# Performance work log

Measured on AMD Instinct MI355X. Metric: run time of the kernel, lower is better.

## Reference

```python
import jax, jax.numpy as jnp
import numpy as np

N = 50000          # nodes
DEG = 8            # per-node in/out degree
E = N * DEG        # fwd edges (rev = reversed fwd)
H = 128            # hidden_dim
T = 4              # towers
F = H // T         # per-tower F_in (divide_input=True)
FO = H // T        # per-tower F_out
L = 2              # num_layers
IN_DIM = 128
OUT_DIM = 32
AVG_LOG = float(np.log(DEG + 1.0))  # avg of log(deg+1) from deg histogram (all deg==8)
BN_EPS = 1e-5
STD_EPS = 1e-5


def setup_inputs() -> dict:
    key = jax.random.key(0)
    ks = jax.random.split(key, 10)
    x = jax.random.normal(ks[0], (N, IN_DIM), jnp.float32)
    # every node appears exactly DEG times as dst and as src -> deg histogram delta at 8
    dst = jnp.repeat(jnp.arange(N, dtype=jnp.int32), DEG)
    src = jax.random.permutation(ks[1], dst)
    edge_fwd = jnp.stack([src, dst])  # [2, E]

    def rn(k, shape):
        return jax.random.normal(k, shape, jnp.float32) * 0.05

    return dict(
        x=x,
        W_in=rn(ks[2], (IN_DIM, H)), b_in=jnp.zeros((H,), jnp.float32),
        # [layer, relation(fwd/rev), tower, ...]
        pre_W=rn(ks[3], (L, 2, T, 2 * F, F)), pre_b=jnp.zeros((L, 2, T, F), jnp.float32),
        post_W=rn(ks[4], (L, 2, T, 13 * F, FO)), post_b=jnp.zeros((L, 2, T, FO), jnp.float32),
        lin_W=rn(ks[5], (L, 2, H, H)), lin_b=jnp.zeros((L, 2, H), jnp.float32),
        bn_gamma=jnp.ones((L, H), jnp.float32), bn_beta=jnp.zeros((L, H), jnp.float32),
        mlp_W1=rn(ks[6], (H, H)), mlp_b1=jnp.zeros((H,), jnp.float32),
        mlp_W2=rn(ks[7], (H, OUT_DIM)), mlp_b2=jnp.zeros((OUT_DIM,), jnp.float32),
        edge_fwd=edge_fwd,
    )


def _pna(x, src, dst, pre_W, pre_b, post_W, post_b, lin_W, lin_b):
    """One PNAConv (divide_input=True, pre/post_layers=1, no edge attr)."""
    xt = x.reshape(N, T, F)                                   # [N,T,F]
    # message: cat([x_i (dst), x_j (src)]) -> per-tower pre-MLP
    h = jnp.concatenate([xt[dst], xt[src]], axis=-1)          # [E,T,2F]
    m = jnp.einsum('etf,tfg->etg', h, pre_W) + pre_b          # [E,T,F]
    # multi-aggregator scatter reduce over destination nodes
    deg = jax.ops.segment_sum(jnp.ones((m.shape[0],), x.dtype), dst, N)
    degc = jnp.maximum(deg, 1.0)
    inv = (1.0 / degc)[:, None, None]
    mean = jax.ops.segment_sum(m, dst, N) * inv
    mean2 = jax.ops.segment_sum(m * m, dst, N) * inv
    std = jnp.sqrt(jax.nn.relu(mean2 - mean * mean) + STD_EPS)
    mn = jax.ops.segment_min(m, dst, N)
    mx = jax.ops.segment_max(m, dst, N)
    agg = jnp.concatenate([mean, mn, mx, std], axis=-1)       # [N,T,4F]
    # degree scalers: amplification, attenuation, identity
    ld = jnp.log(degc + 1.0)[:, None, None]
    agg = jnp.concatenate([agg * (ld / AVG_LOG), agg * (AVG_LOG / ld), agg], axis=-1)  # [N,T,12F]
    out = jnp.concatenate([xt, agg], axis=-1)                 # [N,T,13F]
    out = jnp.einsum('ntf,tfg->ntg', out, post_W) + post_b    # [N,T,FO]
    out = out.reshape(N, T * FO)
    return out @ lin_W + lin_b                                # [N,H]


def _bn(x, g, b):
    mu = x.mean(0)
    var = x.var(0)  # biased, as torch BatchNorm normalization
    return g * (x - mu) * jax.lax.rsqrt(var + BN_EPS) + b


def reference(x, W_in, b_in, pre_W, pre_b, post_W, post_b, lin_W, lin_b,
              bn_gamma, bn_beta, mlp_W1, mlp_b1, mlp_W2, mlp_b2, edge_fwd):
    src, dst = edge_fwd[0], edge_fwd[1]
    h = jax.nn.relu(x @ W_in + b_in)
    for l in range(L):
        # HeteroConv sum of fwd relation and rev relation (reversed edges)
        y = (_pna(h, src, dst, pre_W[l, 0], pre_b[l, 0], post_W[l, 0], post_b[l, 0], lin_W[l, 0], lin_b[l, 0])
             + _pna(h, dst, src, pre_W[l, 1], pre_b[l, 1], post_W[l, 1], post_b[l, 1], lin_W[l, 1], lin_b[l, 1]))
        h = jax.nn.relu(_bn(y, bn_gamma[l], bn_beta[l]))
        # dropout omitted (deterministic reference / eval mode)
    return jax.nn.relu(h @ mlp_W1 + mlp_b1) @ mlp_W2 + mlp_b2
```

## Files before the change

kernel.cpp:

```cpp
#include <hip/hip_runtime.h>
#include <hip/hip_fp16.h>
#include <cstddef>
#include <cstdint>

#define NN 50000
#define DEG 8
#define EE (NN*DEG)
#define RT_CNT 3125
#define KSTEPS 36
#define W8L 18432
#define MPAD 132

typedef __attribute__((ext_vector_type(8))) short short8;
typedef __attribute__((ext_vector_type(4))) float f32x4;

union Pack8 { __half h[8]; __half2 h2[4]; uint4 u; short8 s8; };

__global__ void k_build_nbr(const int* __restrict__ ef, int* __restrict__ cnt,
                            int* __restrict__ fwd_nbr, int* __restrict__ rev_nbr) {
    int e = blockIdx.x * blockDim.x + threadIdx.x;
    if (e >= EE) return;
    int s = ef[e], d = ef[EE + e];
    int p = atomicAdd(&cnt[d], 1);
    fwd_nbr[d * DEG + p] = s;
    int q = atomicAdd(&cnt[NN + s], 1);
    rev_nbr[s * DEG + q] = d;
}

__global__ __launch_bounds__(256) void k_wprep(
    const float* __restrict__ post_W, const float* __restrict__ pre_W,
    const float* __restrict__ pre_b, const float* __restrict__ post_b,
    const float* __restrict__ lin_W, const float* __restrict__ lin_b,
    __half* __restrict__ Wcp, float* __restrict__ Qw, float* __restrict__ bc) {
    __shared__ float Pf[160 * 33];
    __shared__ float Wl[32 * 128];
    __shared__ float Wt[32 * 32];
    __shared__ float Ps[32 * 32];
    __shared__ float Q[32 * 32];
    __shared__ float T3s[32];
    int tid = threadIdx.x;
    int m4 = blockIdx.x;
    int l = m4 >> 3, r = (m4 >> 2) & 1, tw = m4 & 3;
    const float* PW = post_W + (size_t)m4 * 416 * 32;
    for (int i = tid; i < 160 * 32; i += 256) {
        int row = i >> 5, g = i & 31;
        float v;
        if (row < 32) v = PW[row * 32 + g];
        else {
            int rr = row - 32;
            v = PW[(32 + rr) * 32 + g] + PW[(160 + rr) * 32 + g] + PW[(288 + rr) * 32 + g];
        }
        Pf[row * 33 + g] = v;
    }
    for (int i = tid; i < 1024; i += 256) Wt[i] = pre_W[(size_t)m4 * 2048 + i];
    for (int i = tid; i < 4096; i += 256)
        Wl[i] = lin_W[(size_t)(l * 2 + r) * 16384 + tw * 32 * 128 + i];
    __syncthreads();
    for (int i = tid; i < 1024; i += 256) {
        int g = i >> 5, j = i & 31;
        Ps[i] = Pf[(32 + g) * 33 + j] + Pf[(64 + g) * 33 + j] + Pf[(96 + g) * 33 + j];
    }
    __syncthreads();
    for (int i = tid; i < 1024; i += 256) {
        int f = i >> 5, j = i & 31;
        float acc = Pf[f * 33 + j];
#pragma unroll
        for (int g = 0; g < 32; g++) acc += Wt[f * 32 + g] * Ps[g * 32 + j];
        Q[i] = acc;
    }
    if (tid < 32) {
        int j = tid;
        float v = post_b[m4 * 32 + j];
#pragma unroll
        for (int g = 0; g < 32; g++) v += pre_b[m4 * 32 + g] * Ps[g * 32 + j];
        T3s[j] = v;
    }
    __syncthreads();
    for (int u = tid; u < 2048; u += 256) {
        int lane = u & 63, t = (u >> 6) & 7, s = u >> 9;
        int quad = lane >> 4, nl = lane & 15;
        int n = t * 16 + nl;
        Pack8 pk;
#pragma unroll
        for (int e = 0; e < 8; e++) {
            int f = quad * 8 + e;
            const float* Pr = &Pf[((s + 1) * 32 + f) * 33];
            float acc = 0.f;
#pragma unroll
            for (int j = 0; j < 32; j++) acc += Pr[j] * Wl[j * 128 + n];
            pk.h[e] = __float2half(acc);
        }
        int ks = 4 + r * 16 + tw * 4 + s;
        *(uint4*)&Wcp[((size_t)l * W8L + (t * KSTEPS + ks) * 64 + lane) * 8] = pk.u;
    }
    for (int i = tid; i < 4096; i += 256) {
        int f = i >> 7, n = i & 127;
        float acc = 0.f;
#pragma unroll
        for (int j = 0; j < 32; j++) acc += Q[f * 32 + j] * Wl[j * 128 + n];
        atomicAdd(&Qw[(size_t)l * 16384 + (tw * 32 + f) * 128 + n], acc);
    }
    if (tid < 128) {
        float v = 0.f;
#pragma unroll
        for (int j = 0; j < 32; j++) v += T3s[j] * Wl[j * 128 + tid];
        atomicAdd(&bc[l * 128 + tid], v);
        if ((m4 & 7) == 0)
            atomicAdd(&bc[l * 128 + tid],
                      lin_b[(2 * l) * 128 + tid] + lin_b[(2 * l + 1) * 128 + tid]);
    }
}

__global__ void k_pack_xt(const float* __restrict__ Qw, __half* __restrict__ Wcp) {
    int gid = blockIdx.x * blockDim.x + threadIdx.x;
    if (gid >= 2 * 4 * 8 * 64) return;
    int lane = gid & 63, t = (gid >> 6) & 7, ks = (gid >> 9) & 3, l = gid >> 11;
    int quad = lane >> 4;
    int n = t * 16 + (lane & 15);
    Pack8 pk;
#pragma unroll
    for (int e = 0; e < 8; e++)
        pk.h[e] = __float2half(Qw[(size_t)l * 16384 + (ks * 32 + quad * 8 + e) * 128 + n]);
    *(uint4*)&Wcp[((size_t)l * W8L + (t * KSTEPS + ks) * 64 + lane) * 8] = pk.u;
}

__global__ void k_pack_b(const float* __restrict__ W, int K, int N,
                         __half* __restrict__ dst) {
    int gid = blockIdx.x * blockDim.x + threadIdx.x;
    int total = (K >> 5) * (N >> 4) * 64;
    if (gid >= total) return;
    int lane = gid & 63;
    int ks = (gid >> 6) % (K >> 5);
    int t = (gid >> 6) / (K >> 5);
    int quad = lane >> 4, nl = lane & 15;
    int n = t * 16 + nl;
    Pack8 pk;
#pragma unroll
    for (int e = 0; e < 8; e++)
        pk.h[e] = __float2half(W[(size_t)(ks * 32 + quad * 8 + e) * N + n]);
    *(uint4*)&dst[(size_t)gid * 8] = pk.u;
}

__global__ void k_pack_wbd(const float* __restrict__ pre_W, __half* __restrict__ dst) {
    int gid = blockIdx.x * blockDim.x + threadIdx.x;
    if (gid >= 2 * 2 * 8 * 4 * 64) return;
    int lane = gid & 63, ks = (gid >> 6) & 3, t8 = (gid >> 8) & 7;
    int rel = (gid >> 11) & 1, l = gid >> 12;
    int quad = lane >> 4, nl = lane & 15;
    int n = t8 * 16 + nl;
    int tn = n >> 5;
    Pack8 pk;
#pragma unroll
    for (int e = 0; e < 8; e++) {
        int k = ks * 32 + quad * 8 + e;
        float v = 0.f;
        if ((k >> 5) == tn)
            v = pre_W[(size_t)((((l * 2 + rel) * 4 + tn) * 64) + 32 + (k & 31)) * 32 + (n & 31)];
        pk.h[e] = __float2half(v);
    }
    *(uint4*)&dst[((size_t)(l * 2 + rel) * 2048 + (t8 * 4 + ks) * 64 + lane) * 8] = pk.u;
}

__global__ __launch_bounds__(256) void k_in_fused(
    const float* __restrict__ X, const __half* __restrict__ Wp,
    const float* __restrict__ b, const __half* __restrict__ WbBDp,
    __half* __restrict__ H, __half* __restrict__ Bplanes) {
    __shared__ __half Sh[4][16 * MPAD];
    int tid = threadIdx.x, wv = tid >> 6, lane = tid & 63;
    int rt = blockIdx.x * 4 + wv;
    if (rt >= RT_CNT) rt = RT_CNT - 1;
    int mm = lane & 15, quad = lane >> 4;
    short8 a[4];
#pragma unroll
    for (int ks = 0; ks < 4; ks++) {
        const float4* p = (const float4*)&X[(size_t)(rt * 16 + mm) * 128 + ks * 32 + quad * 8];
        float4 v0 = p[0], v1 = p[1];
        Pack8 pk;
        pk.h[0] = __float2half(v0.x); pk.h[1] = __float2half(v0.y);
        pk.h[2] = __float2half(v0.z); pk.h[3] = __float2half(v0.w);
        pk.h[4] = __float2half(v1.x); pk.h[5] = __float2half(v1.y);
        pk.h[6] = __float2half(v1.z); pk.h[7] = __float2half(v1.w);
        a[ks] = pk.s8;
    }
    const short8* Bb = (const short8*)Wp + lane;
    f32x4 acc[8];
#pragma unroll
    for (int t = 0; t < 8; t++) acc[t] = (f32x4){0.f, 0.f, 0.f, 0.f};
#pragma unroll
    for (int ks = 0; ks < 4; ks++)
#pragma unroll
        for (int t = 0; t < 8; t++)
            acc[t] = __builtin_amdgcn_mfma_f32_16x16x32_f16(
                a[ks], Bb[(t * 4 + ks) * 64], acc[t], 0, 0, 0);
    __half* T = Sh[wv];
#pragma unroll
    for (int t = 0; t < 8; t++) {
        int n = t * 16 + mm;
        float bias = b[n];
#pragma unroll
        for (int r = 0; r < 4; r++)
            T[(quad * 4 + r) * MPAD + n] = __float2half(fmaxf(acc[t][r] + bias, 0.f));
    }
#pragma unroll
    for (int it = 0; it < 4; it++) {
        int idx = it * 64 + lane;
        int row = idx >> 4, col = (idx & 15) * 8;
        *(uint4*)&H[(size_t)(rt * 16 + row) * 128 + col] = *(uint4*)&T[row * MPAD + col];
    }
    short8 a2[4];
#pragma unroll
    for (int ks = 0; ks < 4; ks++)
        a2[ks] = *(const short8*)&T[mm * MPAD + ks * 32 + quad * 8];
#pragma unroll
    for (int rel = 0; rel < 2; rel++) {
        const short8* Bd = (const short8*)WbBDp + (size_t)rel * 2048 + lane;
        f32x4 ac[8];
#pragma unroll
        for (int t = 0; t < 8; t++) ac[t] = (f32x4){0.f, 0.f, 0.f, 0.f};
#pragma unroll
        for (int ks = 0; ks < 4; ks++)
#pragma unroll
            for (int t = 0; t < 8; t++)
                ac[t] = __builtin_amdgcn_mfma_f32_16x16x32_f16(
                    a2[ks], Bd[(t * 4 + ks) * 64], ac[t], 0, 0, 0);
#pragma unroll
        for (int t = 0; t < 8; t++) {
            int n = t * 16 + mm;
#pragma unroll
            for (int r = 0; r < 4; r++)
                T[(quad * 4 + r) * MPAD + n] = __float2half(ac[t][r]);
        }
        __half* Bp = Bplanes + (size_t)rel * NN * 128;
#pragma unroll
        for (int it = 0; it < 4; it++) {
            int idx = it * 64 + lane;
            int row = idx >> 4, col = (idx & 15) * 8;
            *(uint4*)&Bp[(size_t)(rt * 16 + row) * 128 + col] = *(uint4*)&T[row * MPAD + col];
        }
    }
}

template<int V>
__global__ __launch_bounds__(256) void k_preB_mfma(
    const __half* __restrict__ Hin, const float* __restrict__ Yf,
    const float* __restrict__ bns, const float* __restrict__ bns2,
    const float* __restrict__ gamma, const float* __restrict__ beta,
    __half* __restrict__ Hout, const __half* __restrict__ WbBDp,
    __half* __restrict__ Bplanes) {
    __shared__ __half Sh[4][16 * MPAD];
    __shared__ float sc[128], sh[128];
    int tid = threadIdx.x, wv = tid >> 6, lane = tid & 63;
    int rt = blockIdx.x * 4 + wv;
    if (rt >= RT_CNT) rt = RT_CNT - 1;
    if (V == 2) {
        if (tid < 128) {
            float mu = bns[tid] * (1.f / NN);
            float var = bns2[tid] * (1.f / NN) - mu * mu;
            float s = gamma[tid] * rsqrtf(var + 1e-5f);
            sc[tid] = s;
            sh[tid] = beta[tid] - mu * s;
        }
        __syncthreads();
    }
    int mm = lane & 15, quad = lane >> 4;
    short8 a[4];
#pragma unroll
    for (int ks = 0; ks < 4; ks++) {
        int c0 = ks * 32 + quad * 8;
        size_t base = (size_t)(rt * 16 + mm) * 128 + c0;
        if (V == 1) {
            Pack8 pk; pk.u = *(const uint4*)&Hin[base];
            a[ks] = pk.s8;
        } else {
            const float4* p = (const float4*)&Yf[base];
            float4 v0 = p[0], v1 = p[1];
            float4 s0 = *(const float4*)&sc[c0], s1 = *(const float4*)&sc[c0 + 4];
            float4 f0 = *(const float4*)&sh[c0], f1 = *(const float4*)&sh[c0 + 4];
            Pack8 pk;
            pk.h[0] = __float2half(fmaxf(s0.x * v0.x + f0.x, 0.f));
            pk.h[1] = __float2half(fmaxf(s0.y * v0.y + f0.y, 0.f));
            pk.h[2] = __float2half(fmaxf(s0.z * v0.z + f0.z, 0.f));
            pk.h[3] = __float2half(fmaxf(s0.w * v0.w + f0.w, 0.f));
            pk.h[4] = __float2half(fmaxf(s1.x * v1.x + f1.x, 0.f));
            pk.h[5] = __float2half(fmaxf(s1.y * v1.y + f1.y, 0.f));
            pk.h[6] = __float2half(fmaxf(s1.z * v1.z + f1.z, 0.f));
            pk.h[7] = __float2half(fmaxf(s1.w * v1.w + f1.w, 0.f));
            *(uint4*)&Hout[base] = pk.u;
            a[ks] = pk.s8;
        }
    }
    __half* T = Sh[wv];
#pragma unroll
    for (int rel = 0; rel < 2; rel++) {
        const short8* Bb = (const short8*)WbBDp + (size_t)rel * 2048 + lane;
        f32x4 acc[8];
#pragma unroll
        for (int t = 0; t < 8; t++) acc[t] = (f32x4){0.f, 0.f, 0.f, 0.f};
#pragma unroll
        for (int ks = 0; ks < 4; ks++)
#pragma unroll
            for (int t = 0; t < 8; t++)
                acc[t] = __builtin_amdgcn_mfma_f32_16x16x32_f16(
                    a[ks], Bb[(t * 4 + ks) * 64], acc[t], 0, 0, 0);
#pragma unroll
        for (int t = 0; t < 8; t++) {
            int n = t * 16 + mm;
#pragma unroll
            for (int r = 0; r < 4; r++)
                T[(quad * 4 + r) * MPAD + n] = __float2half(acc[t][r]);
        }
        __half* Bp = Bplanes + (size_t)rel * NN * 128;
#pragma unroll
        for (int it = 0; it < 4; it++) {
            int idx = it * 64 + lane;
            int row = idx >> 4, col = (idx & 15) * 8;
            *(uint4*)&Bp[(size_t)(rt * 16 + row) * 128 + col] = *(uint4*)&T[row * MPAD + col];
        }
    }
}

__global__ __launch_bounds__(256, 5) void k_agg_gemm(
    const __half* __restrict__ hbuf, const __half* __restrict__ Bplanes,
    const int* __restrict__ fwd_nbr, const int* __restrict__ rev_nbr,
    const __half* __restrict__ Wcp, const float* __restrict__ bc,
    float* __restrict__ Y, float* __restrict__ bnsum, float* __restrict__ bnsum2) {
    __shared__ __half Spack[32 * 64 * 8];
    int tid = threadIdx.x;
    int blk = blockIdx.x;
    int lane = tid & 63, wv = tid >> 6;
    int s = lane >> 4, f16 = lane & 15;
    int tw = f16 >> 2, quad = f16 & 3;
    int m = wv * 4 + s;
    int d = blk * 16 + m;
    int mB = lane & 15, qB = lane >> 4;
    Pack8 axt[4];
#pragma unroll
    for (int ks = 0; ks < 4; ks++)
        axt[ks].u = *(const uint4*)&hbuf[(size_t)(blk * 16 + mB) * 128 + ks * 32 + qB * 8];
    {
        const int4* nf = (const int4*)&fwd_nbr[d * 8];
        const int4* nr = (const int4*)&rev_nbr[d * 8];
        int4 a0 = nf[0], a1 = nf[1], b0v = nr[0], b1v = nr[1];
        int idx0[8] = {a0.x, a0.y, a0.z, a0.w, a1.x, a1.y, a1.z, a1.w};
        int idx1[8] = {b0v.x, b0v.y, b0v.z, b0v.w, b1v.x, b1v.y, b1v.z, b1v.w};
        int fo = f16 * 8;
        Pack8 r0[8], r1[8];
        const __half* Bp1 = Bplanes + (size_t)NN * 128;
#pragma unroll
        for (int k = 0; k < 8; k++)
            r0[k].u = *(const uint4*)&Bplanes[(size_t)idx0[k] * 128 + fo];
#pragma unroll
        for (int k = 0; k < 8; k++)
            r1[k].u = *(const uint4*)&Bp1[(size_t)idx1[k] * 128 + fo];
        int pos = 16 * quad + (m ^ quad ^ ((tw & 1) << 2));
#pragma unroll
        for (int rel = 0; rel < 2; rel++) {
            Pack8* rr = rel ? r1 : r0;
            float sS[8], qS[8], mnS[8], mxS[8];
#pragma unroll
            for (int j = 0; j < 8; j++) {
                sS[j] = 0.f; qS[j] = 0.f; mnS[j] = 1e30f; mxS[j] = -1e30f;
            }
#pragma unroll
            for (int k = 0; k < 8; k++) {
#pragma unroll
                for (int j2 = 0; j2 < 4; j2++) {
                    __half2 h = rr[k].h2[j2];
                    float a = __half2float(__low2half(h));
                    float b = __half2float(__high2half(h));
                    int j0 = 2 * j2, j1 = j0 + 1;
                    sS[j0] += a; qS[j0] += a * a;
                    mnS[j0] = fminf(mnS[j0], a); mxS[j0] = fmaxf(mxS[j0], a);
                    sS[j1] += b; qS[j1] += b * b;
                    mnS[j1] = fminf(mnS[j1], b); mxS[j1] = fmaxf(mxS[j1], b);
                }
            }
            Pack8 mean, stdv, mnp, mxp;
#pragma unroll
            for (int j = 0; j < 8; j++) {
                float Bm = sS[j] * 0.125f;
                mean.h[j] = __float2half(Bm);
                stdv.h[j] = __float2half(
                    sqrtf(fmaxf(qS[j] * 0.125f - Bm * Bm, 0.f) + 1e-5f));
                mnp.h[j] = __float2half(mnS[j]);
                mxp.h[j] = __float2half(mxS[j]);
            }
            int ksb = rel * 16 + tw * 4;
            *(uint4*)&Spack[((size_t)(ksb + 0) * 64 + pos) * 8] = mean.u;
            *(uint4*)&Spack[((size_t)(ksb + 1) * 64 + pos) * 8] = mnp.u;
            *(uint4*)&Spack[((size_t)(ksb + 2) * 64 + pos) * 8] = mxp.u;
            *(uint4*)&Spack[((size_t)(ksb + 3) * 64 + pos) * 8] = stdv.u;
        }
    }
    __syncthreads();
    int t0 = wv * 2;
    const short8* Bb = (const short8*)Wcp + lane;
    f32x4 acc0 = (f32x4){0.f, 0.f, 0.f, 0.f};
    f32x4 acc1 = (f32x4){0.f, 0.f, 0.f, 0.f};
    short8 p0[6], p1[6];
#pragma unroll
    for (int dd = 0; dd < 6; dd++) {
        p0[dd] = Bb[((size_t)t0 * KSTEPS + dd) * 64];
        p1[dd] = Bb[((size_t)(t0 + 1) * KSTEPS + dd) * 64];
    }
    __builtin_amdgcn_s_setprio(1);
#pragma unroll
    for (int ks = 0; ks < KSTEPS; ks++) {
        short8 a;
        if (ks < 4) {
            a = axt[ks].s8;
        } else {
            int ss = ks - 4;
            int twk = (ss >> 2) & 3;
            int posr = 16 * qB + (mB ^ qB ^ ((twk & 1) << 2));
            a = *(const short8*)&Spack[((size_t)ss * 64 + posr) * 8];
        }
        acc0 = __builtin_amdgcn_mfma_f32_16x16x32_f16(a, p0[ks % 6], acc0, 0, 0, 0);
        acc1 = __builtin_amdgcn_mfma_f32_16x16x32_f16(a, p1[ks % 6], acc1, 0, 0, 0);
        if (ks + 6 < KSTEPS) {
            p0[ks % 6] = Bb[((size_t)t0 * KSTEPS + ks + 6) * 64];
            p1[ks % 6] = Bb[((size_t)(t0 + 1) * KSTEPS + ks + 6) * 64];
        }
    }
    __builtin_amdgcn_s_setprio(0);
#pragma unroll
    for (int tt = 0; tt < 2; tt++) {
        f32x4 acc = tt ? acc1 : acc0;
        int n = (t0 + tt) * 16 + mB;
        float bias = bc[n];
        float ls = 0.f, ls2 = 0.f;
#pragma unroll
        for (int r = 0; r < 4; r++) {
            float v = acc[r] + bias;
            int node = blk * 16 + qB * 4 + r;
            Y[(size_t)node * 128 + n] = v;
            ls += v; ls2 += v * v;
        }
        ls += __shfl_xor(ls, 16); ls += __shfl_xor(ls, 32);
        ls2 += __shfl_xor(ls2, 16); ls2 += __shfl_xor(ls2, 32);
        if (qB == 0) {
            atomicAdd(&bnsum[n], ls);
            atomicAdd(&bnsum2[n], ls2);
        }
    }
}

__global__ __launch_bounds__(256) void k_mlp_mfma(
    const float* __restrict__ Yb, const float* __restrict__ bns,
    const float* __restrict__ bns2, const float* __restrict__ gamma,
    const float* __restrict__ beta, const __half* __restrict__ W1p,
    const float* __restrict__ b1, const __half* __restrict__ W2p,
    const float* __restrict__ b2, float* __restrict__ out) {
    __shared__ __half Sh[4][16 * MPAD];
    __shared__ float sc[128], sh[128];
    int tid = threadIdx.x, wv = tid >> 6, lane = tid & 63;
    int rt = blockIdx.x * 4 + wv;
    if (rt >= RT_CNT) rt = RT_CNT - 1;
    if (tid < 128) {
        float mu = bns[tid] * (1.f / NN);
        float var = bns2[tid] * (1.f / NN) - mu * mu;
        float s = gamma[tid] * rsqrtf(var + 1e-5f);
        sc[tid] = s;
        sh[tid] = beta[tid] - mu * s;
    }
    __syncthreads();
    int mm = lane & 15, quad = lane >> 4;
    short8 a[4];
#pragma unroll
    for (int ks = 0; ks < 4; ks++) {
        int c0 = ks * 32 + quad * 8;
        const float4* p = (const float4*)&Yb[(size_t)(rt * 16 + mm) * 128 + c0];
        float4 v0 = p[0], v1 = p[1];
        float4 s0 = *(const float4*)&sc[c0], s1 = *(const float4*)&sc[c0 + 4];
        float4 f0 = *(const float4*)&sh[c0], f1 = *(const float4*)&sh[c0 + 4];
        Pack8 pk;
        pk.h[0] = __float2half(fmaxf(s0.x * v0.x + f0.x, 0.f));
        pk.h[1] = __float2half(fmaxf(s0.y * v0.y + f0.y, 0.f));
        pk.h[2] = __float2half(fmaxf(s0.z * v0.z + f0.z, 0.f));
        pk.h[3] = __float2half(fmaxf(s0.w * v0.w + f0.w, 0.f));
        pk.h[4] = __float2half(fmaxf(s1.x * v1.x + f1.x, 0.f));
        pk.h[5] = __float2half(fmaxf(s1.y * v1.y + f1.y, 0.f));
        pk.h[6] = __float2half(fmaxf(s1.z * v1.z + f1.z, 0.f));
        pk.h[7] = __float2half(fmaxf(s1.w * v1.w + f1.w, 0.f));
        a[ks] = pk.s8;
    }
    const short8* B1 = (const short8*)W1p + lane;
    f32x4 acc[8];
#pragma unroll
    for (int t = 0; t < 8; t++) acc[t] = (f32x4){0.f, 0.f, 0.f, 0.f};
#pragma unroll
    for (int ks = 0; ks < 4; ks++)
#pragma unroll
        for (int t = 0; t < 8; t++)
            acc[t] = __builtin_amdgcn_mfma_f32_16x16x32_f16(
                a[ks], B1[(t * 4 + ks) * 64], acc[t], 0, 0, 0);
    __half* T = Sh[wv];
#pragma unroll
    for (int t = 0; t < 8; t++) {
        int n = t * 16 + mm;
        float bias = b1[n];
#pragma unroll
        for (int r = 0; r < 4; r++)
            T[(quad * 4 + r) * MPAD + n] = __float2half(fmaxf(acc[t][r] + bias, 0.f));
    }
    short8 a2[4];
#pragma unroll
    for (int ks = 0; ks < 4; ks++)
        a2[ks] = *(const short8*)&T[mm * MPAD + ks * 32 + quad * 8];
    const short8* B2 = (const short8*)W2p + lane;
    f32x4 acc2[2];
#pragma unroll
    for (int t = 0; t < 2; t++) acc2[t] = (f32x4){0.f, 0.f, 0.f, 0.f};
#pragma unroll
    for (int ks = 0; ks < 4; ks++)
#pragma unroll
        for (int t = 0; t < 2; t++)
            acc2[t] = __builtin_amdgcn_mfma_f32_16x16x32_f16(
                a2[ks], B2[(t * 4 + ks) * 64], acc2[t], 0, 0, 0);
#pragma unroll
    for (int t = 0; t < 2; t++) {
        int n = t * 16 + mm;
        float bias = b2[n];
#pragma unroll
        for (int r = 0; r < 4; r++)
            out[(size_t)(rt * 16 + quad * 4 + r) * 32 + n] = acc2[t][r] + bias;
    }
}

extern "C" void kernel_launch(void* const* d_in, const int* in_sizes, int n_in,
                              void* d_out, int out_size, void* d_ws, size_t ws_size,
                              hipStream_t stream) {
    const float* x      = (const float*)d_in[0];
    const float* W_in   = (const float*)d_in[1];
    const float* b_in   = (const float*)d_in[2];
    const float* pre_W  = (const float*)d_in[3];
    const float* pre_b  = (const float*)d_in[4];
    const float* post_W = (const float*)d_in[5];
    const float* post_b = (const float*)d_in[6];
    const float* lin_W  = (const float*)d_in[7];
    const float* lin_b  = (const float*)d_in[8];
    const float* bn_g   = (const float*)d_in[9];
    const float* bn_b   = (const float*)d_in[10];
    const float* mlp_W1 = (const float*)d_in[11];
    const float* mlp_b1 = (const float*)d_in[12];
    const float* mlp_W2 = (const float*)d_in[13];
    const float* mlp_b2 = (const float*)d_in[14];
    const int*   edge   = (const int*)d_in[15];
    float* out = (float*)d_out;

    char* w = (char*)d_ws;
    const size_t plane = (size_t)NN * 128 * sizeof(float);
    __half* hbuf = (__half*)w; w += plane / 2;
    float* ybuf = (float*)w; w += plane;
    __half* Bpl = (__half*)w; w += plane;
    int* fwd_nbr = (int*)w; w += (size_t)NN * DEG * sizeof(int);
    int* rev_nbr = (int*)w; w += (size_t)NN * DEG * sizeof(int);
    int* cnt     = (int*)w; w += (size_t)2 * NN * sizeof(int);
    float* Qw    = (float*)w; w += (size_t)2 * 128 * 128 * sizeof(float);
    float* bc    = (float*)w; w += 2 * 128 * sizeof(float);
    __half* Wcp  = (__half*)w; w += (size_t)2 * KSTEPS * 32 * 128 * sizeof(__half);
    __half* Winp = (__half*)w; w += (size_t)128 * 128 * sizeof(__half);
    __half* W1p  = (__half*)w; w += (size_t)128 * 128 * sizeof(__half);
    __half* W2p  = (__half*)w; w += (size_t)128 * 32 * sizeof(__half);
    __half* WbBD = (__half*)w; w += (size_t)4 * 128 * 128 * sizeof(__half);
    float* bns   = (float*)w; w += 4 * 128 * sizeof(float);

    const int gWave = (RT_CNT + 3) / 4;

    (void)hipMemsetAsync(cnt, 0, (size_t)2 * NN * sizeof(int), stream);
    (void)hipMemsetAsync(Qw, 0, (size_t)(2 * 128 * 128 + 2 * 128) * sizeof(float), stream);
    (void)hipMemsetAsync(bns, 0, 4 * 128 * sizeof(float), stream);
    k_build_nbr<<<(EE + 255) / 256, 256, 0, stream>>>(edge, cnt, fwd_nbr, rev_nbr);
    k_wprep<<<16, 256, 0, stream>>>(post_W, pre_W, pre_b, post_b, lin_W, lin_b,
                                    Wcp, Qw, bc);
    k_pack_xt<<<16, 256, 0, stream>>>(Qw, Wcp);
    k_pack_b<<<8, 256, 0, stream>>>(W_in, 128, 128, Winp);
    k_pack_b<<<8, 256, 0, stream>>>(mlp_W1, 128, 128, W1p);
    k_pack_b<<<2, 256, 0, stream>>>(mlp_W2, 128, 32, W2p);
    k_pack_wbd<<<32, 256, 0, stream>>>(pre_W, WbBD);

    k_in_fused<<<gWave, 256, 0, stream>>>(x, Winp, b_in, WbBD, hbuf, Bpl);

    k_agg_gemm<<<RT_CNT, 256, 0, stream>>>(
        hbuf, Bpl, fwd_nbr, rev_nbr, Wcp, bc, ybuf, bns, bns + 128);
    k_preB_mfma<2><<<gWave, 256, 0, stream>>>(
        nullptr, ybuf, bns, bns + 128, bn_g, bn_b, hbuf,
        WbBD + (size_t)2 * 128 * 128, Bpl);
    k_agg_gemm<<<RT_CNT, 256, 0, stream>>>(
        hbuf, Bpl, fwd_nbr, rev_nbr, Wcp + (size_t)KSTEPS * 32 * 128,
        bc + 128, ybuf, bns + 256, bns + 384);

    k_mlp_mfma<<<gWave, 256, 0, stream>>>(ybuf, bns + 256, bns + 384,
                                          bn_g + 128, bn_b + 128,
                                          W1p, mlp_b1, W2p, mlp_b2, out);
}
```

Measured before the change: 454.9 us.

## Make agg-gemm persistent with double-buffered LDS and prefetched neighbor gathers

The aggregation+GEMM kernel becomes a persistent kernel: 512 blocks of 512 threads loop over the 16-node tiles with a stride equal to the grid size. While one tile's MFMA GEMM runs, the neighbor gather for the next tile is already issued, and its statistics go into a second LDS buffer. Each wave now does one output column tile instead of two, and fwd/rev gathers are spread across half-waves. The aim is to hide gather latency behind the GEMM and cut per-block launch and prologue cost. In exchange the kernel runs fewer resident blocks, uses twice the LDS per block, and tiles are split unevenly across the grid (3125 tiles over 512 blocks).

```diff
diff --git a/kernel.cpp b/kernel.cpp
--- a/kernel.cpp
+++ b/kernel.cpp
@@ -10,6 +10,7 @@
 #define KSTEPS 36
 #define W8L 18432
 #define MPAD 132
+#define GRID_B2 512
 
 typedef __attribute__((ext_vector_type(8))) short short8;
 typedef __attribute__((ext_vector_type(4))) float f32x4;
@@ -319,129 +320,131 @@
     }
 }
 
-__global__ __launch_bounds__(256, 5) void k_agg_gemm(
+__device__ __forceinline__ void gather_issue(const __half* __restrict__ P,
+                                             const int* __restrict__ nbr,
+                                             int tile, int nloc, int fo, Pack8* rn) {
+    const int4* np = (const int4*)&nbr[(tile * 16 + nloc) * 8];
+    int4 i0 = np[0], i1 = np[1];
+    int idx[8] = {i0.x, i0.y, i0.z, i0.w, i1.x, i1.y, i1.z, i1.w};
+#pragma unroll
+    for (int k = 0; k < 8; k++)
+        rn[k].u = *(const uint4*)&P[(size_t)idx[k] * 128 + fo];
+}
+
+__device__ __forceinline__ void stats_store(const Pack8* rn, __half* __restrict__ Sp,
+                                            int ksb, int pos) {
+    float sS[8], qS[8], mnS[8], mxS[8];
+#pragma unroll
+    for (int j = 0; j < 8; j++) {
+        sS[j] = 0.f; qS[j] = 0.f; mnS[j] = 1e30f; mxS[j] = -1e30f;
+    }
+#pragma unroll
+    for (int k = 0; k < 8; k++) {
+#pragma unroll
+        for (int j2 = 0; j2 < 4; j2++) {
+            __half2 h = rn[k].h2[j2];
+            float a = __half2float(__low2half(h));
+            float b = __half2float(__high2half(h));
+            int j0 = 2 * j2, j1 = j0 + 1;
+            sS[j0] += a; qS[j0] += a * a;
+            mnS[j0] = fminf(mnS[j0], a); mxS[j0] = fmaxf(mxS[j0], a);
+            sS[j1] += b; qS[j1] += b * b;
+            mnS[j1] = fminf(mnS[j1], b); mxS[j1] = fmaxf(mxS[j1], b);
+        }
+    }
+    Pack8 mean, stdv, mnp, mxp;
+#pragma unroll
+    for (int j = 0; j < 8; j++) {
+        float Bm = sS[j] * 0.125f;
+        mean.h[j] = __float2half(Bm);
+        stdv.h[j] = __float2half(sqrtf(fmaxf(qS[j] * 0.125f - Bm * Bm, 0.f) + 1e-5f));
+        mnp.h[j] = __float2half(mnS[j]);
+        mxp.h[j] = __float2half(mxS[j]);
+    }
+    *(uint4*)&Sp[((size_t)(ksb + 0) * 64 + pos) * 8] = mean.u;
+    *(uint4*)&Sp[((size_t)(ksb + 1) * 64 + pos) * 8] = mnp.u;
+    *(uint4*)&Sp[((size_t)(ksb + 2) * 64 + pos) * 8] = mxp.u;
+    *(uint4*)&Sp[((size_t)(ksb + 3) * 64 + pos) * 8] = stdv.u;
+}
+
+__global__ __launch_bounds__(512, 4) void k_agg_gemm(
     const __half* __restrict__ hbuf, const __half* __restrict__ Bplanes,
     const int* __restrict__ fwd_nbr, const int* __restrict__ rev_nbr,
     const __half* __restrict__ Wcp, const float* __restrict__ bc,
     float* __restrict__ Y, float* __restrict__ bnsum, float* __restrict__ bnsum2) {
-    __shared__ __half Spack[32 * 64 * 8];
-    int tid = threadIdx.x;
-    int blk = blockIdx.x;
-    int lane = tid & 63, wv = tid >> 6;
-    int s = lane >> 4, f16 = lane & 15;
+    __shared__ __half Spack[2][32 * 64 * 8];
+    int tid = threadIdx.x, lane = tid & 63, wv = tid >> 6;
+    int g = lane >> 4, f16 = lane & 15;
+    int nloc = wv * 2 + (g >> 1);
+    int rel = g & 1;
+    const int* nbr = rel ? rev_nbr : fwd_nbr;
+    const __half* Pl = rel ? (Bplanes + (size_t)NN * 128) : Bplanes;
+    int fo = f16 * 8;
     int tw = f16 >> 2, quad = f16 & 3;
-    int m = wv * 4 + s;
-    int d = blk * 16 + m;
+    int pos = 16 * quad + (nloc ^ quad ^ ((tw & 1) << 2));
+    int ksb = rel * 16 + tw * 4;
     int mB = lane & 15, qB = lane >> 4;
-    Pack8 axt[4];
+    int t = wv;
+    const short8* Bb = (const short8*)Wcp + lane;
+    float bias = bc[t * 16 + mB];
+
+    int tile = blockIdx.x;
+    Pack8 rn[8], axt[4];
+    gather_issue(Pl, nbr, tile, nloc, fo, rn);
 #pragma unroll
     for (int ks = 0; ks < 4; ks++)
-        axt[ks].u = *(const uint4*)&hbuf[(size_t)(blk * 16 + mB) * 128 + ks * 32 + qB * 8];
-    {
-        const int4* nf = (const int4*)&fwd_nbr[d * 8];
-        const int4* nr = (const int4*)&rev_nbr[d * 8];
-        int4 a0 = nf[0], a1 = nf[1], b0v = nr[0], b1v = nr[1];
-        int idx0[8] = {a0.x, a0.y, a0.z, a0.w, a1.x, a1.y, a1.z, a1.w};
-        int idx1[8] = {b0v.x, b0v.y, b0v.z, b0v.w, b1v.x, b1v.y, b1v.z, b1v.w};
-        int fo = f16 * 8;
-        Pack8 r0[8], r1[8];
-        const __half* Bp1 = Bplanes + (size_t)NN * 128;
-#pragma unroll
-        for (int k = 0; k < 8; k++)
-            r0[k].u = *(const uint4*)&Bplanes[(size_t)idx0[k] * 128 + fo];
-#pragma unroll
-        for (int k = 0; k < 8; k++)
-            r1[k].u = *(const uint4*)&Bp1[(size_t)idx1[k] * 128 + fo];
-        int pos = 16 * quad + (m ^ quad ^ ((tw & 1) << 2));
-#pragma unroll
-        for (int rel = 0; rel < 2; rel++) {
-            Pack8* rr = rel ? r1 : r0;
-            float sS[8], qS[8], mnS[8], mxS[8];
-#pragma unroll
-            for (int j = 0; j < 8; j++) {
-                sS[j] = 0.f; qS[j] = 0.f; mnS[j] = 1e30f; mxS[j] = -1e30f;
+        axt[ks].u = *(const uint4*)&hbuf[(size_t)(tile * 16 + mB) * 128 + ks * 32 + qB * 8];
+    stats_store(rn, Spack[0], ksb, pos);
+    __syncthreads();
+    int buf = 0;
+    while (true) {
+        int nxt = tile + GRID_B2;
+        bool hn = nxt < RT_CNT;
+        if (hn) gather_issue(Pl, nbr, nxt, nloc, fo, rn);
+        f32x4 acc = (f32x4){0.f, 0.f, 0.f, 0.f};
+        short8 p[6];
+#pragma unroll
+        for (int dd = 0; dd < 6; dd++) p[dd] = Bb[((size_t)t * KSTEPS + dd) * 64];
+        __builtin_amdgcn_s_setprio(1);
+#pragma unroll
+        for (int ks = 0; ks < KSTEPS; ks++) {
+            short8 a;
+            if (ks < 4) {
+                a = axt[ks].s8;
+            } else {
+                int ss = ks - 4;
+                int twk = (ss >> 2) & 3;
+                int posr = 16 * qB + (mB ^ qB ^ ((twk & 1) << 2));
+                a = *(const short8*)&Spack[buf][((size_t)ss * 64 + posr) * 8];
             }
-#pragma unroll
-            for (int k = 0; k < 8; k++) {
-#pragma unroll
-                for (int j2 = 0; j2 < 4; j2++) {
-                    __half2 h = rr[k].h2[j2];
-                    float a = __half2float(__low2half(h));
-                    float b = __half2float(__high2half(h));
-                    int j0 = 2 * j2, j1 = j0 + 1;
-                    sS[j0] += a; qS[j0] += a * a;
-                    mnS[j0] = fminf(mnS[j0], a); mxS[j0] = fmaxf(mxS[j0], a);
-                    sS[j1] += b; qS[j1] += b * b;
-                    mnS[j1] = fminf(mnS[j1], b); mxS[j1] = fmaxf(mxS[j1], b);
-                }
+            acc = __builtin_amdgcn_mfma_f32_16x16x32_f16(a, p[ks % 6], acc, 0, 0, 0);
+            if (ks + 6 < KSTEPS) p[ks % 6] = Bb[((size_t)t * KSTEPS + ks + 6) * 64];
+        }
+        __builtin_amdgcn_s_setprio(0);
+        {
+            int n = t * 16 + mB;
+            float ls = 0.f, ls2 = 0.f;
+#pragma unroll
+            for (int r = 0; r < 4; r++) {
+                float v = acc[r] + bias;
+                Y[(size_t)(tile * 16 + qB * 4 + r) * 128 + n] = v;
+                ls += v; ls2 += v * v;
             }
-            Pack8 mean, stdv, mnp, mxp;
-#pragma unroll
-            for (int j = 0; j < 8; j++) {
-                float Bm = sS[j] * 0.125f;
-                mean.h[j] = __float2half(Bm);
-                stdv.h[j] = __float2half(
-                    sqrtf(fmaxf(qS[j] * 0.125f - Bm * Bm, 0.f) + 1e-5f));
-                mnp.h[j] = __float2half(mnS[j]);
-                mxp.h[j] = __float2half(mxS[j]);
+            ls += __shfl_xor(ls, 16); ls += __shfl_xor(ls, 32);
+            ls2 += __shfl_xor(ls2, 16); ls2 += __shfl_xor(ls2, 32);
+            if (qB == 0) {
+                atomicAdd(&bnsum[n], ls);
+                atomicAdd(&bnsum2[n], ls2);
             }
-            int ksb = rel * 16 + tw * 4;
-            *(uint4*)&Spack[((size_t)(ksb + 0) * 64 + pos) * 8] = mean.u;
-            *(uint4*)&Spack[((size_t)(ksb + 1) * 64 + pos) * 8] = mnp.u;
-            *(uint4*)&Spack[((size_t)(ksb + 2) * 64 + pos) * 8] = mxp.u;
-            *(uint4*)&Spack[((size_t)(ksb + 3) * 64 + pos) * 8] = stdv.u;
-        }
-    }
-    __syncthreads();
-    int t0 = wv * 2;
-    const short8* Bb = (const short8*)Wcp + lane;
-    f32x4 acc0 = (f32x4){0.f, 0.f, 0.f, 0.f};
-    f32x4 acc1 = (f32x4){0.f, 0.f, 0.f, 0.f};
-    short8 p0[6], p1[6];
-#pragma unroll
-    for (int dd = 0; dd < 6; dd++) {
-        p0[dd] = Bb[((size_t)t0 * KSTEPS + dd) * 64];
-        p1[dd] = Bb[((size_t)(t0 + 1) * KSTEPS + dd) * 64];
-    }
-    __builtin_amdgcn_s_setprio(1);
-#pragma unroll
-    for (int ks = 0; ks < KSTEPS; ks++) {
-        short8 a;
-        if (ks < 4) {
-            a = axt[ks].s8;
-        } else {
-            int ss = ks - 4;
-            int twk = (ss >> 2) & 3;
-            int posr = 16 * qB + (mB ^ qB ^ ((twk & 1) << 2));
-            a = *(const short8*)&Spack[((size_t)ss * 64 + posr) * 8];
-        }
-        acc0 = __builtin_amdgcn_mfma_f32_16x16x32_f16(a, p0[ks % 6], acc0, 0, 0, 0);
-        acc1 = __builtin_amdgcn_mfma_f32_16x16x32_f16(a, p1[ks % 6], acc1, 0, 0, 0);
-        if (ks + 6 < KSTEPS) {
-            p0[ks % 6] = Bb[((size_t)t0 * KSTEPS + ks + 6) * 64];
-            p1[ks % 6] = Bb[((size_t)(t0 + 1) * KSTEPS + ks + 6) * 64];
-        }
-    }
-    __builtin_amdgcn_s_setprio(0);
-#pragma unroll
-    for (int tt = 0; tt < 2; tt++) {
-        f32x4 acc = tt ? acc1 : acc0;
-        int n = (t0 + tt) * 16 + mB;
-        float bias = bc[n];
-        float ls = 0.f, ls2 = 0.f;
-#pragma unroll
-        for (int r = 0; r < 4; r++) {
-            float v = acc[r] + bias;
-            int node = blk * 16 + qB * 4 + r;
-            Y[(size_t)node * 128 + n] = v;
-            ls += v; ls2 += v * v;
-        }
-        ls += __shfl_xor(ls, 16); ls += __shfl_xor(ls, 32);
-        ls2 += __shfl_xor(ls2, 16); ls2 += __shfl_xor(ls2, 32);
-        if (qB == 0) {
-            atomicAdd(&bnsum[n], ls);
-            atomicAdd(&bnsum2[n], ls2);
-        }
+        }
+        if (!hn) break;
+#pragma unroll
+        for (int ks = 0; ks < 4; ks++)
+            axt[ks].u = *(const uint4*)&hbuf[(size_t)(nxt * 16 + mB) * 128 + ks * 32 + qB * 8];
+        stats_store(rn, Spack[buf ^ 1], ksb, pos);
+        __syncthreads();
+        buf ^= 1;
+        tile = nxt;
     }
 }
 
@@ -581,12 +584,12 @@
 
     k_in_fused<<<gWave, 256, 0, stream>>>(x, Winp, b_in, WbBD, hbuf, Bpl);
 
-    k_agg_gemm<<<RT_CNT, 256, 0, stream>>>(
+    k_agg_gemm<<<GRID_B2, 512, 0, stream>>>(
         hbuf, Bpl, fwd_nbr, rev_nbr, Wcp, bc, ybuf, bns, bns + 128);
     k_preB_mfma<2><<<gWave, 256, 0, stream>>>(
         nullptr, ybuf, bns, bns + 128, bn_g, bn_b, hbuf,
         WbBD + (size_t)2 * 128 * 128, Bpl);
-    k_agg_gemm<<<RT_CNT, 256, 0, stream>>>(
+    k_agg_gemm<<<GRID_B2, 512, 0, stream>>>(
         hbuf, Bpl, fwd_nbr, rev_nbr, Wcp + (size_t)KSTEPS * 32 * 128,
         bc + 128, ybuf, bns + 256, bns + 384);
 
```

Measured after the change: 642.6 us. 1.41x slower.

## Tile aggregation GEMM as 32 nodes per 512-thread block, one N-tile per wave

Applied to the files above, without the earlier changes.

The fused aggregation+GEMM kernel now processes 32 destination nodes per block with 8 waves instead of 16 nodes with 4 waves. Each wave owns one 16-column output tile and runs two M-tiles, so each loaded weight fragment feeds two MFMAs rather than being loaded twice across waves. This halves global weight traffic per node and the block count, at the cost of doubled LDS, removal of the occupancy hint in launch bounds, and tail guards for the last partial block.

```diff
diff --git a/kernel.cpp b/kernel.cpp
--- a/kernel.cpp
+++ b/kernel.cpp
@@ -7,6 +7,7 @@
 #define DEG 8
 #define EE (NN*DEG)
 #define RT_CNT 3125
+#define AG_CNT 1563
 #define KSTEPS 36
 #define W8L 18432
 #define MPAD 132
@@ -319,31 +320,40 @@
     }
 }
 
-__global__ __launch_bounds__(256, 5) void k_agg_gemm(
+__global__ __launch_bounds__(512) void k_agg_gemm(
     const __half* __restrict__ hbuf, const __half* __restrict__ Bplanes,
     const int* __restrict__ fwd_nbr, const int* __restrict__ rev_nbr,
     const __half* __restrict__ Wcp, const float* __restrict__ bc,
     float* __restrict__ Y, float* __restrict__ bnsum, float* __restrict__ bnsum2) {
-    __shared__ __half Spack[32 * 64 * 8];
+    __shared__ __half Spack[32 * 128 * 8];
     int tid = threadIdx.x;
     int blk = blockIdx.x;
     int lane = tid & 63, wv = tid >> 6;
-    int s = lane >> 4, f16 = lane & 15;
+    int G = tid >> 4;
+    int f16 = tid & 15;
     int tw = f16 >> 2, quad = f16 & 3;
-    int m = wv * 4 + s;
-    int d = blk * 16 + m;
+    int fo = f16 * 8;
+    int pos = quad * 32 + (G ^ quad ^ ((tw & 1) << 2));
     int mB = lane & 15, qB = lane >> 4;
-    Pack8 axt[4];
-#pragma unroll
-    for (int ks = 0; ks < 4; ks++)
-        axt[ks].u = *(const uint4*)&hbuf[(size_t)(blk * 16 + mB) * 128 + ks * 32 + qB * 8];
+    int t = wv;
+    int nodeg = blk * 32 + G;
+    if (nodeg >= NN) nodeg = NN - 1;
+
+    Pack8 axt[2][4];
+#pragma unroll
+    for (int mt = 0; mt < 2; mt++) {
+        int nd = blk * 32 + mt * 16 + mB;
+        if (nd >= NN) nd = NN - 1;
+#pragma unroll
+        for (int ks = 0; ks < 4; ks++)
+            axt[mt][ks].u = *(const uint4*)&hbuf[(size_t)nd * 128 + ks * 32 + qB * 8];
+    }
     {
-        const int4* nf = (const int4*)&fwd_nbr[d * 8];
-        const int4* nr = (const int4*)&rev_nbr[d * 8];
+        const int4* nf = (const int4*)&fwd_nbr[nodeg * 8];
+        const int4* nr = (const int4*)&rev_nbr[nodeg * 8];
         int4 a0 = nf[0], a1 = nf[1], b0v = nr[0], b1v = nr[1];
         int idx0[8] = {a0.x, a0.y, a0.z, a0.w, a1.x, a1.y, a1.z, a1.w};
         int idx1[8] = {b0v.x, b0v.y, b0v.z, b0v.w, b1v.x, b1v.y, b1v.z, b1v.w};
-        int fo = f16 * 8;
         Pack8 r0[8], r1[8];
         const __half* Bp1 = Bplanes + (size_t)NN * 128;
 #pragma unroll
@@ -352,7 +362,6 @@
 #pragma unroll
         for (int k = 0; k < 8; k++)
             r1[k].u = *(const uint4*)&Bp1[(size_t)idx1[k] * 128 + fo];
-        int pos = 16 * quad + (m ^ quad ^ ((tw & 1) << 2));
 #pragma unroll
         for (int rel = 0; rel < 2; rel++) {
             Pack8* rr = rel ? r1 : r0;
@@ -386,55 +395,53 @@
                 mxp.h[j] = __float2half(mxS[j]);
             }
             int ksb = rel * 16 + tw * 4;
-            *(uint4*)&Spack[((size_t)(ksb + 0) * 64 + pos) * 8] = mean.u;
-            *(uint4*)&Spack[((size_t)(ksb + 1) * 64 + pos) * 8] = mnp.u;
-            *(uint4*)&Spack[((size_t)(ksb + 2) * 64 + pos) * 8] = mxp.u;
-            *(uint4*)&Spack[((size_t)(ksb + 3) * 64 + pos) * 8] = stdv.u;
+            *(uint4*)&Spack[((size_t)(ksb + 0) * 128 + pos) * 8] = mean.u;
+            *(uint4*)&Spack[((size_t)(ksb + 1) * 128 + pos) * 8] = mnp.u;
+            *(uint4*)&Spack[((size_t)(ksb + 2) * 128 + pos) * 8] = mxp.u;
+            *(uint4*)&Spack[((size_t)(ksb + 3) * 128 + pos) * 8] = stdv.u;
         }
     }
     __syncthreads();
-    int t0 = wv * 2;
     const short8* Bb = (const short8*)Wcp + lane;
     f32x4 acc0 = (f32x4){0.f, 0.f, 0.f, 0.f};
     f32x4 acc1 = (f32x4){0.f, 0.f, 0.f, 0.f};
-    short8 p0[6], p1[6];
-#pragma unroll
-    for (int dd = 0; dd < 6; dd++) {
-        p0[dd] = Bb[((size_t)t0 * KSTEPS + dd) * 64];
-        p1[dd] = Bb[((size_t)(t0 + 1) * KSTEPS + dd) * 64];
-    }
+    short8 p[6];
+#pragma unroll
+    for (int dd = 0; dd < 6; dd++) p[dd] = Bb[((size_t)t * KSTEPS + dd) * 64];
     __builtin_amdgcn_s_setprio(1);
 #pragma unroll
     for (int ks = 0; ks < KSTEPS; ks++) {
-        short8 a;
+        short8 a0f, a1f;
         if (ks < 4) {
-            a = axt[ks].s8;
+            a0f = axt[0][ks].s8;
+            a1f = axt[1][ks].s8;
         } else {
             int ss = ks - 4;
             int twk = (ss >> 2) & 3;
-            int posr = 16 * qB + (mB ^ qB ^ ((twk & 1) << 2));
-            a = *(const short8*)&Spack[((size_t)ss * 64 + posr) * 8];
-        }
-        acc0 = __builtin_amdgcn_mfma_f32_16x16x32_f16(a, p0[ks % 6], acc0, 0, 0, 0);
-        acc1 = __builtin_amdgcn_mfma_f32_16x16x32_f16(a, p1[ks % 6], acc1, 0, 0, 0);
-        if (ks + 6 < KSTEPS) {
-            p0[ks % 6] = Bb[((size_t)t0 * KSTEPS + ks + 6) * 64];
-            p1[ks % 6] = Bb[((size_t)(t0 + 1) * KSTEPS + ks + 6) * 64];
-        }
+            int posr = qB * 32 + (mB ^ qB ^ ((twk & 1) << 2));
+            const __half* row = &Spack[((size_t)ss * 128 + posr) * 8];
+            a0f = *(const short8*)row;
+            a1f = *(const short8*)(row + 16 * 8);
+        }
+        acc0 = __builtin_amdgcn_mfma_f32_16x16x32_f16(a0f, p[ks % 6], acc0, 0, 0, 0);
+        acc1 = __builtin_amdgcn_mfma_f32_16x16x32_f16(a1f, p[ks % 6], acc1, 0, 0, 0);
+        if (ks + 6 < KSTEPS) p[ks % 6] = Bb[((size_t)t * KSTEPS + ks + 6) * 64];
     }
     __builtin_amdgcn_s_setprio(0);
 #pragma unroll
-    for (int tt = 0; tt < 2; tt++) {
-        f32x4 acc = tt ? acc1 : acc0;
-        int n = (t0 + tt) * 16 + mB;
+    for (int mt = 0; mt < 2; mt++) {
+        f32x4 acc = mt ? acc1 : acc0;
+        int n = t * 16 + mB;
         float bias = bc[n];
         float ls = 0.f, ls2 = 0.f;
 #pragma unroll
         for (int r = 0; r < 4; r++) {
-            float v = acc[r] + bias;
-            int node = blk * 16 + qB * 4 + r;
-            Y[(size_t)node * 128 + n] = v;
-            ls += v; ls2 += v * v;
+            int node = blk * 32 + mt * 16 + qB * 4 + r;
+            if (node < NN) {
+                float v = acc[r] + bias;
+                Y[(size_t)node * 128 + n] = v;
+                ls += v; ls2 += v * v;
+            }
         }
         ls += __shfl_xor(ls, 16); ls += __shfl_xor(ls, 32);
         ls2 += __shfl_xor(ls2, 16); ls2 += __shfl_xor(ls2, 32);
@@ -581,12 +588,12 @@
 
     k_in_fused<<<gWave, 256, 0, stream>>>(x, Winp, b_in, WbBD, hbuf, Bpl);
 
-    k_agg_gemm<<<RT_CNT, 256, 0, stream>>>(
+    k_agg_gemm<<<AG_CNT, 512, 0, stream>>>(
         hbuf, Bpl, fwd_nbr, rev_nbr, Wcp, bc, ybuf, bns, bns + 128);
     k_preB_mfma<2><<<gWave, 256, 0, stream>>>(
         nullptr, ybuf, bns, bns + 128, bn_g, bn_b, hbuf,
         WbBD + (size_t)2 * 128 * 128, Bpl);
-    k_agg_gemm<<<RT_CNT, 256, 0, stream>>>(
+    k_agg_gemm<<<AG_CNT, 512, 0, stream>>>(
         hbuf, Bpl, fwd_nbr, rev_nbr, Wcp + (size_t)KSTEPS * 32 * 128,
         bc + 128, ybuf, bns + 256, bns + 384);
 
```

New measurement: 455.9 us. No clear change (+0.2%).
